# Kernel optimization log

Hardware: AMD Instinct MI355X
Metric: run time of the kernel (lower is better)

The kernel has to match this reference:

```python
import jax, jax.numpy as jnp
import numpy as np

# Config constants (from init_kwargs)
RADIUS_UPDATE_RATE = 0.01
MIN_RADIUS = 0.1
MAX_RADIUS = 2.0
EPS = 1e-6


def _finite(x, fallback):
    """nan/inf guard: replace non-finite entries with fallback (same math as torch.where(isnan|isinf,...))."""
    bad = jnp.isnan(x) | jnp.isinf(x)
    return jnp.where(bad, fallback, x)


def _compute_score(r, causal=True):
    """QuantumAttention.compute_score: relu'd 2-D dot-product interaction,
    causal mask, row-normalized. r: [B,S,2] -> score: [B,S,S]."""
    raw = jnp.einsum('bse,bte->bst', r, r)          # thin bmm, inner dim 2
    score = jax.nn.relu(raw)
    if causal:
        S = r.shape[1]
        mask = jnp.tril(jnp.ones((S, S), dtype=bool))
        score = jnp.where(mask[None, :, :], score, 0.0)
    denom = jnp.clip(jnp.sum(score, axis=-1, keepdims=True), EPS, None)
    return score / denom


def setup_inputs() -> dict:
    key = jax.random.key(0)
    k1, k2 = jax.random.split(key)
    B, S = 4, 4096
    r_embed = jax.random.normal(k1, (B, S, 2), dtype=jnp.float32)
    # dt in a realistic (dt_scale .. dt_max) range
    dt = jax.random.uniform(k2, (B,), dtype=jnp.float32, minval=1e-4, maxval=1e-2)
    return {"r_embed": r_embed, "dt": dt}


def reference(r_embed, dt):
    # Heun-Euler integration step with radius rescale.
    dt_e = dt[:, None, None]                         # [B,1,1]

    # Stage 1 (k1)
    score = _compute_score(r_embed, causal=True)     # [B,S,S]
    context = jnp.einsum('bst,bte->bse', score, r_embed)
    k1 = _finite(dt_e * context, 0.0)
    r_mid = _finite(r_embed + k1, r_embed)

    # Stage 2 (k2)
    score_mid = _compute_score(r_mid, causal=True)
    context_mid = jnp.einsum('bst,bte->bse', score_mid, r_mid)
    k2 = _finite(dt_e * context_mid, 0.0)

    # Final update + radius adjustment
    r_new = r_embed + 0.5 * (k1 + k2)
    new_radius = jnp.clip(jnp.linalg.norm(r_new, axis=-1, keepdims=True), EPS, None)
    radius_adjustment = jnp.sum(score, axis=-1, keepdims=True) * RADIUS_UPDATE_RATE
    adjusted_radius = jnp.clip(new_radius + radius_adjustment, MIN_RADIUS, MAX_RADIUS)
    scale_factor = adjusted_radius / new_radius
    r_final = r_new * scale_factor
    r_final = _finite(r_final, r_embed)
    return r_final, score
```

## Files before the change

kernel.cpp:

```cpp
#include <hip/hip_runtime.h>
#include <math.h>


#define S_LEN 4096
#define ROWS  16384
#define BLK   256
#define EPSF  1e-6f
#define RATE  0.01f
#define MINR  0.1f
#define MAXR  2.0f

__device__ __forceinline__ void reduce3(float &a, float &b, float &c, float* red) {
    #pragma unroll
    for (int off = 32; off > 0; off >>= 1) {
        a += __shfl_down(a, off);
        b += __shfl_down(b, off);
        c += __shfl_down(c, off);
    }
    const int wave = threadIdx.x >> 6;
    if ((threadIdx.x & 63) == 0) { red[wave*3] = a; red[wave*3+1] = b; red[wave*3+2] = c; }
    __syncthreads();
    if (threadIdx.x == 0) {
        a = red[0] + red[3] + red[6] + red[9];
        b = red[1] + red[4] + red[7] + red[10];
        c = red[2] + red[5] + red[8] + red[11];
    }
}


__global__ __launch_bounds__(BLK) void k_pass1(
    const float2* __restrict__ r_in,
    const float* __restrict__ dt_in,
    float* __restrict__ ws,
    float* __restrict__ score_out)
{
    __shared__ float red[12];
    __shared__ float bc[1];

    const int row = blockIdx.x;
    const int b = row >> 12;
    const int s = row & (S_LEN - 1);
    const float2* rb = r_in + ((size_t)b << 12);
    const float4* rb4 = (const float4*)rb;
    const float2 rs = rb[s];

    float dsum = 0.f, nx = 0.f, ny = 0.f;
    for (int i = threadIdx.x; 2*i <= s; i += BLK) {
        float4 p = rb4[i];
        float d0 = fmaxf(rs.x * p.x + rs.y * p.y, 0.f);
        dsum += d0; nx = fmaf(d0, p.x, nx); ny = fmaf(d0, p.y, ny);
        if (2*i + 1 <= s) {
            float d1 = fmaxf(rs.x * p.z + rs.y * p.w, 0.f);
            dsum += d1; nx = fmaf(d1, p.z, nx); ny = fmaf(d1, p.w, ny);
        }
    }
    reduce3(dsum, nx, ny, red);
    if (threadIdx.x == 0) {
        const float D  = dsum;
        const float dc = fmaxf(D, EPSF);
        const float dtb = dt_in[b];
        float k1x = dtb * nx / dc;
        float k1y = dtb * ny / dc;
        if (!isfinite(k1x)) k1x = 0.f;
        if (!isfinite(k1y)) k1y = 0.f;
        float rmx = rs.x + k1x, rmy = rs.y + k1y;
        if (!isfinite(rmx)) rmx = rs.x;
        if (!isfinite(rmy)) rmy = rs.y;
        float* rmid = ws;
        float* k1w  = ws + 2 * ROWS;
        float* s1w  = ws + 4 * ROWS;
        rmid[2*row]   = rmx; rmid[2*row+1] = rmy;
        k1w[2*row]    = k1x; k1w[2*row+1]  = k1y;
        s1w[row]      = D / dc;
        bc[0]         = 1.f / dc;
    }
    __syncthreads();
    const float inv = bc[0];
    const float isx = rs.x * inv, isy = rs.y * inv;

    float* orow = score_out + (size_t)row * S_LEN;
    #pragma unroll
    for (int q = 0; q < 4; q++) {
        const int t0 = (threadIdx.x << 2) + (q << 10);
        float4 v = make_float4(0.f, 0.f, 0.f, 0.f);
        if (t0 <= s) {
            float4 p01 = rb4[t0 >> 1];
            float4 p23 = rb4[(t0 >> 1) + 1];
            v.x = fmaxf(isx * p01.x + isy * p01.y, 0.f);
            v.y = (t0 + 1 <= s) ? fmaxf(isx * p01.z + isy * p01.w, 0.f) : 0.f;
            v.z = (t0 + 2 <= s) ? fmaxf(isx * p23.x + isy * p23.y, 0.f) : 0.f;
            v.w = (t0 + 3 <= s) ? fmaxf(isx * p23.z + isy * p23.w, 0.f) : 0.f;
        }
        *((float4*)(orow + t0)) = v;
    }
}

__global__ __launch_bounds__(BLK) void k_pass2(
    const float2* __restrict__ r_in,
    const float* __restrict__ dt_in,
    const float* __restrict__ ws,
    float* __restrict__ rfinal_out)
{
    __shared__ float red[12];

    const int row = blockIdx.x;
    const int b = row >> 12;
    const int s = row & (S_LEN - 1);
    const float2* rm = ((const float2*)ws) + ((size_t)b << 12);
    const float4* rm4 = (const float4*)rm;
    const float2 rs = rm[s];

    float dsum = 0.f, nx = 0.f, ny = 0.f;
    for (int i = threadIdx.x; 2*i <= s; i += BLK) {
        float4 p = rm4[i];
        float d0 = fmaxf(rs.x * p.x + rs.y * p.y, 0.f);
        dsum += d0; nx = fmaf(d0, p.x, nx); ny = fmaf(d0, p.y, ny);
        if (2*i + 1 <= s) {
            float d1 = fmaxf(rs.x * p.z + rs.y * p.w, 0.f);
            dsum += d1; nx = fmaf(d1, p.z, nx); ny = fmaf(d1, p.w, ny);
        }
    }
    reduce3(dsum, nx, ny, red);
    if (threadIdx.x == 0) {
        const float* k1w = ws + 2 * ROWS;
        const float* s1w = ws + 4 * ROWS;
        const float dc = fmaxf(dsum, EPSF);
        const float dtb = dt_in[b];
        float k2x = dtb * nx / dc;
        float k2y = dtb * ny / dc;
        if (!isfinite(k2x)) k2x = 0.f;
        if (!isfinite(k2y)) k2y = 0.f;
        const float2 r0 = r_in[row];
        const float k1x = k1w[2*row], k1y = k1w[2*row+1];
        const float rnx = r0.x + 0.5f * (k1x + k2x);
        const float rny = r0.y + 0.5f * (k1y + k2y);
        const float nr = fmaxf(sqrtf(rnx*rnx + rny*rny), EPSF);
        const float ar = fminf(fmaxf(nr + s1w[row] * RATE, MINR), MAXR);
        const float sc = ar / nr;
        float fx = rnx * sc, fy = rny * sc;
        if (!isfinite(fx)) fx = r0.x;
        if (!isfinite(fy)) fy = r0.y;
        rfinal_out[2*row]   = fx;
        rfinal_out[2*row+1] = fy;
    }
}

extern "C" void kernel_launch(void* const* d_in, const int* in_sizes, int n_in,
                              void* d_out, int out_size, void* d_ws, size_t ws_size,
                              hipStream_t stream) {
    const float2* r_in  = (const float2*)d_in[0];
    const float*  dt_in = (const float*)d_in[1];
    float* out = (float*)d_out;
    float* ws  = (float*)d_ws;

    float* rfinal_out = out;
    float* score_out  = out + (size_t)2 * ROWS;

    hipLaunchKernelGGL(k_pass1, dim3(ROWS), dim3(BLK), 0, stream,
                       r_in, dt_in, ws, score_out);
    hipLaunchKernelGGL(k_pass2, dim3(ROWS), dim3(BLK), 0, stream,
                       r_in, dt_in, ws, rfinal_out);
}
```

Baseline: 273.4 us.

## Map one row per wavefront and use nontemporal stores for score output

Each 256-thread block now handles four rows, one per 64-lane wavefront. Reductions use only wave shuffles, which removes the shared-memory staging and block-level __syncthreads. The score matrix is written with nontemporal stores so the large write stream does not pollute the cache. In exchange, each wave has to reduce over up to 4096 elements on its own, and per-row work becomes more uneven across waves because of the causal triangle.

Measured after the change: 287.7 us. 5.2% more time.

```diff
diff --git a/kernel.cpp b/kernel.cpp
--- a/kernel.cpp
+++ b/kernel.cpp
@@ -10,20 +10,14 @@
 #define MINR  0.1f
 #define MAXR  2.0f
 
-__device__ __forceinline__ void reduce3(float &a, float &b, float &c, float* red) {
+typedef float vf4 __attribute__((ext_vector_type(4)));
+
+__device__ __forceinline__ void wave_red3(float &a, float &b, float &c) {
     #pragma unroll
     for (int off = 32; off > 0; off >>= 1) {
         a += __shfl_down(a, off);
         b += __shfl_down(b, off);
         c += __shfl_down(c, off);
-    }
-    const int wave = threadIdx.x >> 6;
-    if ((threadIdx.x & 63) == 0) { red[wave*3] = a; red[wave*3+1] = b; red[wave*3+2] = c; }
-    __syncthreads();
-    if (threadIdx.x == 0) {
-        a = red[0] + red[3] + red[6] + red[9];
-        b = red[1] + red[4] + red[7] + red[10];
-        c = red[2] + red[5] + red[8] + red[11];
     }
 }
 
@@ -34,19 +28,17 @@
     float* __restrict__ ws,
     float* __restrict__ score_out)
 {
-    __shared__ float red[12];
-    __shared__ float bc[1];
-
-    const int row = blockIdx.x;
+    const int lane = threadIdx.x & 63;
+    const int row  = (blockIdx.x << 2) + (threadIdx.x >> 6);
     const int b = row >> 12;
     const int s = row & (S_LEN - 1);
-    const float2* rb = r_in + ((size_t)b << 12);
-    const float4* rb4 = (const float4*)rb;
-    const float2 rs = rb[s];
+    const float2* rb  = r_in + ((size_t)b << 12);
+    const vf4*    rb4 = (const vf4*)rb;
+    const float2  rs  = rb[s];
 
     float dsum = 0.f, nx = 0.f, ny = 0.f;
-    for (int i = threadIdx.x; 2*i <= s; i += BLK) {
-        float4 p = rb4[i];
+    for (int i = lane; 2*i <= s; i += 64) {
+        vf4 p = rb4[i];
         float d0 = fmaxf(rs.x * p.x + rs.y * p.y, 0.f);
         dsum += d0; nx = fmaf(d0, p.x, nx); ny = fmaf(d0, p.y, ny);
         if (2*i + 1 <= s) {
@@ -54,13 +46,17 @@
             dsum += d1; nx = fmaf(d1, p.z, nx); ny = fmaf(d1, p.w, ny);
         }
     }
-    reduce3(dsum, nx, ny, red);
-    if (threadIdx.x == 0) {
-        const float D  = dsum;
-        const float dc = fmaxf(D, EPSF);
+    wave_red3(dsum, nx, ny);
+    const float D  = __shfl(dsum, 0);
+    const float Nx = __shfl(nx, 0);
+    const float Ny = __shfl(ny, 0);
+
+    const float dc  = fmaxf(D, EPSF);
+    const float inv = 1.f / dc;
+    if (lane == 0) {
         const float dtb = dt_in[b];
-        float k1x = dtb * nx / dc;
-        float k1y = dtb * ny / dc;
+        float k1x = dtb * Nx * inv;
+        float k1y = dtb * Ny * inv;
         if (!isfinite(k1x)) k1x = 0.f;
         if (!isfinite(k1y)) k1y = 0.f;
         float rmx = rs.x + k1x, rmy = rs.y + k1y;
@@ -71,27 +67,25 @@
         float* s1w  = ws + 4 * ROWS;
         rmid[2*row]   = rmx; rmid[2*row+1] = rmy;
         k1w[2*row]    = k1x; k1w[2*row+1]  = k1y;
-        s1w[row]      = D / dc;
-        bc[0]         = 1.f / dc;
+        s1w[row]      = D * inv;
     }
-    __syncthreads();
-    const float inv = bc[0];
+
     const float isx = rs.x * inv, isy = rs.y * inv;
-
-    float* orow = score_out + (size_t)row * S_LEN;
-    #pragma unroll
-    for (int q = 0; q < 4; q++) {
-        const int t0 = (threadIdx.x << 2) + (q << 10);
-        float4 v = make_float4(0.f, 0.f, 0.f, 0.f);
-        if (t0 <= s) {
-            float4 p01 = rb4[t0 >> 1];
-            float4 p23 = rb4[(t0 >> 1) + 1];
+    vf4* orow = (vf4*)(score_out + (size_t)row * S_LEN);
+    #pragma unroll 4
+    for (int j = 0; j < 16; j++) {
+        const int i4 = lane + (j << 6);
+        const int t  = i4 << 2;
+        vf4 v = {0.f, 0.f, 0.f, 0.f};
+        if (t <= s) {
+            vf4 p01 = rb4[2*i4];
+            vf4 p23 = rb4[2*i4 + 1];
             v.x = fmaxf(isx * p01.x + isy * p01.y, 0.f);
-            v.y = (t0 + 1 <= s) ? fmaxf(isx * p01.z + isy * p01.w, 0.f) : 0.f;
-            v.z = (t0 + 2 <= s) ? fmaxf(isx * p23.x + isy * p23.y, 0.f) : 0.f;
-            v.w = (t0 + 3 <= s) ? fmaxf(isx * p23.z + isy * p23.w, 0.f) : 0.f;
+            v.y = (t + 1 <= s) ? fmaxf(isx * p01.z + isy * p01.w, 0.f) : 0.f;
+            v.z = (t + 2 <= s) ? fmaxf(isx * p23.x + isy * p23.y, 0.f) : 0.f;
+            v.w = (t + 3 <= s) ? fmaxf(isx * p23.z + isy * p23.w, 0.f) : 0.f;
         }
-        *((float4*)(orow + t0)) = v;
+        __builtin_nontemporal_store(v, orow + i4);
     }
 }
 
@@ -101,18 +95,17 @@
     const float* __restrict__ ws,
     float* __restrict__ rfinal_out)
 {
-    __shared__ float red[12];
-
-    const int row = blockIdx.x;
+    const int lane = threadIdx.x & 63;
+    const int row  = (blockIdx.x << 2) + (threadIdx.x >> 6);
     const int b = row >> 12;
     const int s = row & (S_LEN - 1);
-    const float2* rm = ((const float2*)ws) + ((size_t)b << 12);
-    const float4* rm4 = (const float4*)rm;
-    const float2 rs = rm[s];
+    const float2* rm  = ((const float2*)ws) + ((size_t)b << 12);
+    const vf4*    rm4 = (const vf4*)rm;
+    const float2  rs  = rm[s];
 
     float dsum = 0.f, nx = 0.f, ny = 0.f;
-    for (int i = threadIdx.x; 2*i <= s; i += BLK) {
-        float4 p = rm4[i];
+    for (int i = lane; 2*i <= s; i += 64) {
+        vf4 p = rm4[i];
         float d0 = fmaxf(rs.x * p.x + rs.y * p.y, 0.f);
         dsum += d0; nx = fmaf(d0, p.x, nx); ny = fmaf(d0, p.y, ny);
         if (2*i + 1 <= s) {
@@ -120,8 +113,8 @@
             dsum += d1; nx = fmaf(d1, p.z, nx); ny = fmaf(d1, p.w, ny);
         }
     }
-    reduce3(dsum, nx, ny, red);
-    if (threadIdx.x == 0) {
+    wave_red3(dsum, nx, ny);
+    if (lane == 0) {
         const float* k1w = ws + 2 * ROWS;
         const float* s1w = ws + 4 * ROWS;
         const float dc = fmaxf(dsum, EPSF);
@@ -156,8 +149,8 @@
     float* rfinal_out = out;
     float* score_out  = out + (size_t)2 * ROWS;
 
-    hipLaunchKernelGGL(k_pass1, dim3(ROWS), dim3(BLK), 0, stream,
+    hipLaunchKernelGGL(k_pass1, dim3(ROWS / 4), dim3(BLK), 0, stream,
                        r_in, dt_in, ws, score_out);
-    hipLaunchKernelGGL(k_pass2, dim3(ROWS), dim3(BLK), 0, stream,
+    hipLaunchKernelGGL(k_pass2, dim3(ROWS / 4), dim3(BLK), 0, stream,
                        r_in, dt_in, ws, rfinal_out);
 }
```
